# Optimization experiments

Measured on AMD Instinct MI355X. Metric: run time of the kernel, lower is better.

Reference implementation:

```python
import jax, jax.numpy as jnp
import numpy as np

NUM_NODES = 127   # complete binary tree of depth 7: parent(i) = (i-1)//2
BATCH = 262144
DEPTH = 7


def _project(p):
    """DAG min-propagation in topological order, vectorized per tree level.

    Equivalent to: for parent in topo_order: for child in children(parent):
        p[:, child] = min(p[:, child], p[:, parent])
    Each child has exactly one parent, and parents are always processed before
    children when sweeping levels top-down, so level-parallel updates match the
    edge-sequential reference exactly.
    """
    for level in range(1, DEPTH):
        start, end = 2 ** level - 1, 2 ** (level + 1) - 1
        idx = jnp.arange(start, end)          # children at this level
        par = (idx - 1) // 2                  # their unique parents
        p = p.at[:, idx].set(jnp.minimum(p[:, idx], p[:, par]))
    return p


def setup_inputs() -> dict:
    key = jax.random.key(0)
    x = jax.random.normal(key, (BATCH, NUM_NODES), dtype=jnp.float32)
    return {"x": x}


def reference(x):
    # DAGConstraintLayer.forward: sigmoid then hard DAG projection
    return _project(jax.nn.sigmoid(x))
```

## Files before the change

### kernel.cpp

```cpp
#include <hip/hip_runtime.h>


#define NODES 127u

__global__ __launch_bounds__(256) void DAGConstraintLayer_kernel(
        const float* __restrict__ x, float* __restrict__ out, unsigned total) {
    unsigned e = blockIdx.x * 256u + threadIdx.x;
    if (e >= total) return;

    unsigned b = e / NODES;
    unsigned i = e - b * NODES;
    const float* __restrict__ row = x + (size_t)b * NODES;

    float v = row[i];
    unsigned j = i;
    #pragma unroll
    for (int d = 0; d < 6; ++d) {
        j = j ? (j - 1u) >> 1 : 0u;
        v = fminf(v, row[j]);
    }

    out[e] = 1.0f / (1.0f + __expf(-v));
}

extern "C" void kernel_launch(void* const* d_in, const int* in_sizes, int n_in,
                              void* d_out, int out_size, void* d_ws, size_t ws_size,
                              hipStream_t stream) {
    const float* x = (const float*)d_in[0];
    float* out = (float*)d_out;
    unsigned total = (unsigned)in_sizes[0];
    unsigned grid = (total + 255u) / 256u;
    DAGConstraintLayer_kernel<<<grid, 256, 0, stream>>>(x, out, total);
}
```

Baseline: 268.9 us.

## Use wave-per-row pointer-jumping with shuffles instead of per-element ancestor loads

Each 64-lane wave now owns a row and each lane holds two adjacent nodes, loaded as a float2. The ancestor minimum is computed in three pointer-jumping rounds (ancestor distances 1, 2, 4) using cross-lane shuffles, replacing six redundant global loads per element. A fixed-size grid-stride loop covers all rows. This removes the repeated ancestor reads and the integer division, at the cost of shuffle work and unaligned 8-byte accesses, since rows are 127 floats and odd rows start at odd offsets.

```diff
diff --git a/kernel.cpp b/kernel.cpp
--- a/kernel.cpp
+++ b/kernel.cpp
@@ -1,26 +1,66 @@
 #include <hip/hip_runtime.h>
 
 
-#define NODES 127u
+#define NODES 127
+#define BLOCK 256
+#define GRID  2048
 
-__global__ __launch_bounds__(256) void DAGConstraintLayer_kernel(
-        const float* __restrict__ x, float* __restrict__ out, unsigned total) {
-    unsigned e = blockIdx.x * 256u + threadIdx.x;
-    if (e >= total) return;
+typedef float f2 __attribute__((ext_vector_type(2), aligned(4)));
 
-    unsigned b = e / NODES;
-    unsigned i = e - b * NODES;
-    const float* __restrict__ row = x + (size_t)b * NODES;
+__global__ __launch_bounds__(BLOCK) void dag_kernel(const float* __restrict__ x,
+                                                    float* __restrict__ out,
+                                                    int rows) {
+    const int lane  = threadIdx.x & 63;
+    const int wave  = blockIdx.x * (BLOCK / 64) + (threadIdx.x >> 6);
+    const int nwave = GRID * (BLOCK / 64);
 
-    float v = row[i];
-    unsigned j = i;
+    const int n0 = 2 * lane, n1 = 2 * lane + 1;
+
+    int sl[3][2], cm[3][2];
     #pragma unroll
-    for (int d = 0; d < 6; ++d) {
-        j = j ? (j - 1u) >> 1 : 0u;
-        v = fminf(v, row[j]);
+    for (int r = 0; r < 3; ++r) {
+        const int d = 1 << r;
+        int t0 = (n0 + 1) >> d; int a0 = t0 ? t0 - 1 : 0;
+        int t1 = (n1 + 1) >> d; int a1 = t1 ? t1 - 1 : 0;
+        sl[r][0] = a0 >> 1; cm[r][0] = a0 & 1;
+        sl[r][1] = a1 >> 1; cm[r][1] = a1 & 1;
     }
 
-    out[e] = 1.0f / (1.0f + __expf(-v));
+    for (int r = wave; r < rows; r += nwave) {
+        const float* row = x + (size_t)r * NODES;
+        float vx, vy;
+        if (lane < 63) {
+            f2 t = *(const f2*)(row + n0);
+            vx = t.x; vy = t.y;
+        } else {
+            vx = row[126];
+            vy = __builtin_inff();
+        }
+
+        #pragma unroll
+        for (int rd = 0; rd < 3; ++rd) {
+            float ax = vx, ay = vy;
+            float g0x = __shfl(ax, sl[rd][0]);
+            float g0y = __shfl(ay, sl[rd][0]);
+            float g1x = __shfl(ax, sl[rd][1]);
+            float g1y = __shfl(ay, sl[rd][1]);
+            float p0 = cm[rd][0] ? g0y : g0x;
+            float p1 = cm[rd][1] ? g1y : g1x;
+            vx = fminf(vx, p0);
+            vy = fminf(vy, p1);
+        }
+
+        float sx = 1.0f / (1.0f + __expf(-vx));
+        float sy = 1.0f / (1.0f + __expf(-vy));
+
+        float* orow = out + (size_t)r * NODES;
+        if (lane < 63) {
+            f2 t; t.x = sx; t.y = sy;
+            *(f2*)(orow + n0) = t;
+        } else {
+            orow[126] = sx;
+        }
+    }
 }
 
 extern "C" void kernel_launch(void* const* d_in, const int* in_sizes, int n_in,
@@ -28,7 +68,6 @@
                               hipStream_t stream) {
     const float* x = (const float*)d_in[0];
     float* out = (float*)d_out;
-    unsigned total = (unsigned)in_sizes[0];
-    unsigned grid = (total + 255u) / 256u;
-    DAGConstraintLayer_kernel<<<grid, 256, 0, stream>>>(x, out, total);
+    int rows = in_sizes[0] / NODES;
+    dag_kernel<<<GRID, BLOCK, 0, stream>>>(x, out, rows);
 }
```

Result: faster. 241.0 us (-10.4%).

## Stage row tiles in LDS and propagate min down subtrees per thread

Applied to the files above, without the earlier changes.

Each block now loads 32 rows into shared memory with float4 copies, and eight threads per row each walk one depth-3 subtree recursively, carrying the running min so ancestors are not re-read. Results are written back into shared memory and stored with coalesced float4 writes. This replaces the per-element kernel that gathered six ancestors through global memory for every output. The kernel assumes the row count divides evenly by 32, drops the bounds check, and relies on alignment for the float4 casts. Work is also unevenly spread, since one thread per row handles the top seven nodes.

```diff
diff --git a/kernel.cpp b/kernel.cpp
--- a/kernel.cpp
+++ b/kernel.cpp
@@ -1,26 +1,72 @@
 #include <hip/hip_runtime.h>
 
 
-#define NODES 127u
+#define NODES 127
+#define RPB   32
+#define BLOCK 256
+#define TILE_F4 (RPB * NODES / 4)
 
-__global__ __launch_bounds__(256) void DAGConstraintLayer_kernel(
-        const float* __restrict__ x, float* __restrict__ out, unsigned total) {
-    unsigned e = blockIdx.x * 256u + threadIdx.x;
-    if (e >= total) return;
+__device__ __forceinline__ float sigf(float v) {
+    return 1.0f / (1.0f + __expf(-v));
+}
 
-    unsigned b = e / NODES;
-    unsigned i = e - b * NODES;
-    const float* __restrict__ row = x + (size_t)b * NODES;
+template<int D>
+__device__ __forceinline__ void visit(float* __restrict__ buf, int o, int n, float pm) {
+    float v = fminf(pm, buf[o + n]);
+    buf[o + n] = sigf(v);
+    if constexpr (D > 1) {
+        visit<D - 1>(buf, o, 2 * n + 1, v);
+        visit<D - 1>(buf, o, 2 * n + 2, v);
+    }
+}
 
-    float v = row[i];
-    unsigned j = i;
+__global__ __launch_bounds__(BLOCK, 8) void dag_kernel(const float* __restrict__ x,
+                                                       float* __restrict__ out) {
+    __shared__ float buf[RPB * NODES];
+
+    const size_t base = (size_t)blockIdx.x * (RPB * NODES);
+
+    const float4* __restrict__ src = (const float4*)(x + base);
+    float4* __restrict__ b4 = (float4*)buf;
+    int t = threadIdx.x;
     #pragma unroll
-    for (int d = 0; d < 6; ++d) {
-        j = j ? (j - 1u) >> 1 : 0u;
-        v = fminf(v, row[j]);
+    for (int k = 0; k < 3; ++k) b4[t + k * BLOCK] = src[t + k * BLOCK];
+    if (t + 3 * BLOCK < TILE_F4) b4[t + 3 * BLOCK] = src[t + 3 * BLOCK];
+    __syncthreads();
+
+    const int rl = t >> 3;
+    const int s  = t & 7;
+    const int o  = rl * NODES;
+    const int m3 = 7 + s;
+    const int m2 = (m3 - 1) >> 1;
+    const int m1 = (m2 - 1) >> 1;
+
+    float x0 = buf[o];
+    float a1 = buf[o + m1];
+    float a2 = buf[o + m2];
+
+    if (s == 0) {
+        float X2 = buf[o + 2], X4 = buf[o + 4];
+        float X5 = buf[o + 5], X6 = buf[o + 6];
+        float p1 = fminf(x0, a1);
+        float p2 = fminf(x0, X2);
+        buf[o + 0] = sigf(x0);
+        buf[o + 1] = sigf(p1);
+        buf[o + 2] = sigf(p2);
+        buf[o + 3] = sigf(fminf(p1, a2));
+        buf[o + 4] = sigf(fminf(p1, X4));
+        buf[o + 5] = sigf(fminf(p2, X5));
+        buf[o + 6] = sigf(fminf(p2, X6));
     }
 
-    out[e] = 1.0f / (1.0f + __expf(-v));
+    float pm = fminf(fminf(x0, a1), a2);
+    visit<4>(buf, o, m3, pm);
+    __syncthreads();
+
+    float4* __restrict__ dst = (float4*)(out + base);
+    #pragma unroll
+    for (int k = 0; k < 3; ++k) dst[t + k * BLOCK] = b4[t + k * BLOCK];
+    if (t + 3 * BLOCK < TILE_F4) dst[t + 3 * BLOCK] = b4[t + 3 * BLOCK];
 }
 
 extern "C" void kernel_launch(void* const* d_in, const int* in_sizes, int n_in,
@@ -28,7 +74,7 @@
                               hipStream_t stream) {
     const float* x = (const float*)d_in[0];
     float* out = (float*)d_out;
-    unsigned total = (unsigned)in_sizes[0];
-    unsigned grid = (total + 255u) / 256u;
-    DAGConstraintLayer_kernel<<<grid, 256, 0, stream>>>(x, out, total);
+    int rows = in_sizes[0] / NODES;
+    int grid = rows / RPB;
+    dag_kernel<<<grid, BLOCK, 0, stream>>>(x, out);
 }
```

Result: faster. 230.1 us (-14.5%).

## Stage rows in LDS via direct global-to-LDS loads and propagate per subtree

Applied to the files above, without the earlier changes.

Each wavefront copies 8 full rows into LDS with 16-byte global_load_lds transfers. Eight lanes per row then each handle one depth-3 subtree in registers, compute the min chain and sigmoid, and write back to LDS. Rows are stored out with nontemporal vector stores. This replaces seven scattered, redundant global reads per element with coalesced vector traffic. In exchange, the kernel drops all bounds checks and assumes the row count is a multiple of 32; it also relies on the hardware exp2/rcp approximations.

```diff
diff --git a/kernel.cpp b/kernel.cpp
--- a/kernel.cpp
+++ b/kernel.cpp
@@ -1,26 +1,99 @@
 #include <hip/hip_runtime.h>
 
 
-#define NODES 127u
+#define NODES 127
+#define RPW   8
+#define WPB   4
+#define RPB   (RPW * WPB)
+#define BLOCK 256
+#define WF4   ((RPW * NODES) / 4)
 
-__global__ __launch_bounds__(256) void DAGConstraintLayer_kernel(
-        const float* __restrict__ x, float* __restrict__ out, unsigned total) {
-    unsigned e = blockIdx.x * 256u + threadIdx.x;
-    if (e >= total) return;
+typedef float v4 __attribute__((ext_vector_type(4)));
+typedef const __attribute__((address_space(1))) v4* gp4;
+typedef __attribute__((address_space(3))) v4* lp4;
 
-    unsigned b = e / NODES;
-    unsigned i = e - b * NODES;
-    const float* __restrict__ row = x + (size_t)b * NODES;
+__device__ __forceinline__ float sigf(float v) {
+    float e = __builtin_amdgcn_exp2f(v * -1.44269504089f);
+    return __builtin_amdgcn_rcpf(1.0f + e);
+}
 
-    float v = row[i];
-    unsigned j = i;
+__global__ __launch_bounds__(BLOCK) void dag_kernel(const float* __restrict__ x,
+                                                    float* __restrict__ out) {
+    __shared__ float buf[RPB * NODES];
+    v4* b4 = (v4*)buf;
+
+    const int t    = threadIdx.x;
+    const int lane = t & 63;
+    const int w    = t >> 6;
+    const size_t blk = (size_t)blockIdx.x * (RPB * NODES);
+    const v4* src4 = (const v4*)(x + blk);
+    v4*       dst4 = (v4*)(out + blk);
+    const int wf4 = w * WF4;
+
     #pragma unroll
-    for (int d = 0; d < 6; ++d) {
-        j = j ? (j - 1u) >> 1 : 0u;
-        v = fminf(v, row[j]);
+    for (int k = 0; k < 3; ++k) {
+        int idx = wf4 + k * 64 + lane;
+        __builtin_amdgcn_global_load_lds((gp4)(src4 + idx), (lp4)(b4 + idx), 16, 0, 0);
     }
+    if (lane < 62) {
+        int idx = wf4 + 192 + lane;
+        __builtin_amdgcn_global_load_lds((gp4)(src4 + idx), (lp4)(b4 + idx), 16, 0, 0);
+    }
+    __builtin_amdgcn_s_waitcnt(0x0F70);
 
-    out[e] = 1.0f / (1.0f + __expf(-v));
+    const int r = lane >> 3;
+    const int s = lane & 7;
+    const int o = w * (RPW * NODES) + r * NODES;
+
+    float x0 = buf[o + 0], x1 = buf[o + 1], x2 = buf[o + 2], x3 = buf[o + 3];
+    float x4 = buf[o + 4], x5 = buf[o + 5], x6 = buf[o + 6];
+    float r3  = buf[o + 7 + s];
+    float r40 = buf[o + 15 + 2 * s], r41 = buf[o + 16 + 2 * s];
+    float r50 = buf[o + 31 + 4 * s], r51 = buf[o + 32 + 4 * s];
+    float r52 = buf[o + 33 + 4 * s], r53 = buf[o + 34 + 4 * s];
+    float r60 = buf[o + 63 + 8 * s], r61 = buf[o + 64 + 8 * s];
+    float r62 = buf[o + 65 + 8 * s], r63 = buf[o + 66 + 8 * s];
+    float r64 = buf[o + 67 + 8 * s], r65 = buf[o + 68 + 8 * s];
+    float r66 = buf[o + 69 + 8 * s], r67 = buf[o + 70 + 8 * s];
+
+    float p1 = fminf(x0, x1), p2 = fminf(x0, x2);
+    float p3 = fminf(p1, x3), p4 = fminf(p1, x4);
+    float p5 = fminf(p2, x5), p6 = fminf(p2, x6);
+
+    float pa = (s & 4) ? ((s & 2) ? p6 : p5) : ((s & 2) ? p4 : p3);
+
+    float v3  = fminf(pa, r3);
+    float v40 = fminf(v3, r40),  v41 = fminf(v3, r41);
+    float v50 = fminf(v40, r50), v51 = fminf(v40, r51);
+    float v52 = fminf(v41, r52), v53 = fminf(v41, r53);
+    float v60 = fminf(v50, r60), v61 = fminf(v50, r61);
+    float v62 = fminf(v51, r62), v63 = fminf(v51, r63);
+    float v64 = fminf(v52, r64), v65 = fminf(v52, r65);
+    float v66 = fminf(v53, r66), v67 = fminf(v53, r67);
+
+    buf[o + 7 + s]      = sigf(v3);
+    buf[o + 15 + 2 * s] = sigf(v40);  buf[o + 16 + 2 * s] = sigf(v41);
+    buf[o + 31 + 4 * s] = sigf(v50);  buf[o + 32 + 4 * s] = sigf(v51);
+    buf[o + 33 + 4 * s] = sigf(v52);  buf[o + 34 + 4 * s] = sigf(v53);
+    buf[o + 63 + 8 * s] = sigf(v60);  buf[o + 64 + 8 * s] = sigf(v61);
+    buf[o + 65 + 8 * s] = sigf(v62);  buf[o + 66 + 8 * s] = sigf(v63);
+    buf[o + 67 + 8 * s] = sigf(v64);  buf[o + 68 + 8 * s] = sigf(v65);
+    buf[o + 69 + 8 * s] = sigf(v66);  buf[o + 70 + 8 * s] = sigf(v67);
+
+    float ta = (s & 1) ? ((s & 2) ? p3 : p1) : ((s & 2) ? p2 : x0);
+    float tb = (s & 1) ? p5 : ((s & 2) ? p6 : p4);
+    float vt = (s & 4) ? tb : ta;
+    if (s < 7) buf[o + s] = sigf(vt);
+
+    #pragma unroll
+    for (int k = 0; k < 3; ++k) {
+        int idx = wf4 + k * 64 + lane;
+        __builtin_nontemporal_store(b4[idx], dst4 + idx);
+    }
+    if (lane < 62) {
+        int idx = wf4 + 192 + lane;
+        __builtin_nontemporal_store(b4[idx], dst4 + idx);
+    }
 }
 
 extern "C" void kernel_launch(void* const* d_in, const int* in_sizes, int n_in,
@@ -28,7 +101,7 @@
                               hipStream_t stream) {
     const float* x = (const float*)d_in[0];
     float* out = (float*)d_out;
-    unsigned total = (unsigned)in_sizes[0];
-    unsigned grid = (total + 255u) / 256u;
-    DAGConstraintLayer_kernel<<<grid, 256, 0, stream>>>(x, out, total);
+    int rows = in_sizes[0] / NODES;
+    int grid = rows / RPB;
+    dag_kernel<<<grid, BLOCK, 0, stream>>>(x, out);
 }
```

New measurement: 235.7 us. 12.4% less time.
